# Optimization experiments

Hardware: AMD Instinct MI355X
Metric: run time of the kernel (lower is better)

The kernel has to match this reference:

```python
import jax, jax.numpy as jnp
import numpy as np

NUM_BINS = 4
SCALE = 5.0
EPS = 1e-12

def hswish(x):
    return x * jnp.clip(x + 3.0, 0.0, 6.0) / 6.0

def l2norm(x, axis):
    n = jnp.sqrt(jnp.sum(x * x, axis=axis, keepdims=True))
    return x / jnp.maximum(n, EPS)

def setup_inputs() -> dict:
    key = jax.random.key(0)
    k0, k1, k2, k3, k4 = jax.random.split(key, 5)
    B, C, T, H, W = 8, 256, 32, 28, 28
    hidden, embd = 512, 32
    x = jax.random.normal(k0, (B, C, T, H, W), dtype=jnp.float32)
    W1 = jax.random.normal(k1, (hidden, C), dtype=jnp.float32) * (1.0 / np.sqrt(C))
    b1 = jax.random.normal(k2, (hidden,), dtype=jnp.float32) * 0.01
    W2 = jax.random.normal(k3, (embd, hidden), dtype=jnp.float32) * (1.0 / np.sqrt(hidden))
    b2 = jax.random.normal(k4, (embd,), dtype=jnp.float32) * 0.01
    return {"x": x, "W1": W1, "b1": b1, "W2": W2, "b2": b2}

def reference(x, W1, b1, W2, b2):
    B, C, T, H, W = x.shape
    # encoder: global spatial avg-pool -> 1x1x1 conv -> HSwish -> 1x1x1 conv
    pooled = jnp.mean(x, axis=(3, 4))                      # (B,C,T)
    h = hswish(jnp.einsum('hc,bct->bht', W1, pooled) + b1[None, :, None])
    embds = jnp.einsum('eh,bht->bet', W2, h) + b2[None, :, None]   # (B,E,T)
    norm_embd = l2norm(embds, axis=1)

    # --- grouping (no-grad in original) ---
    ns = jnp.sum(norm_embd[:, :, 1:] * norm_embd[:, :, :-1], axis=1)    # (B,T-1)
    # k-th smallest neighbour similarity = threshold
    smallest = -jax.lax.top_k(-ns, NUM_BINS - 1)[0]                      # ascending smallest k
    threshold = smallest[:, -1]
    edges = (ns > threshold[:, None]).astype(jnp.int32)                  # (B,T-1)
    interval_ends = jnp.concatenate(
        [jnp.zeros((B, 1), dtype=jnp.int32), 1 - edges], axis=1)        # (B,T)
    groups = jnp.cumsum(interval_ends, axis=1)                           # (B,T)
    group_ids = jnp.arange(NUM_BINS, dtype=groups.dtype)
    group_mask = (groups[:, :, None] == group_ids[None, None, :]).astype(jnp.float32)  # (B,T,K)
    group_sizes = jnp.sum(group_mask, axis=1, keepdims=True)             # (B,1,K)
    centers_sum = jnp.einsum('bet,btk->bek', norm_embd, group_mask)      # (B,E,K)
    norm_centers = l2norm(centers_sum / group_sizes, axis=1)             # (B,E,K)
    norm_centers = jax.lax.stop_gradient(norm_centers)

    similarities = jnp.einsum('bet,bek->btk', norm_embd, norm_centers)   # (B,T,K)
    weights = jax.nn.softmax(SCALE * similarities, axis=2)               # (B,T,K)
    sum_weights = jnp.sum(weights, axis=1, keepdims=True)                # (B,1,K)
    scales = jnp.where(sum_weights > 0.0, 1.0 / sum_weights, jnp.ones_like(sum_weights))
    scales = jax.lax.stop_gradient(scales)
    norm_weights = scales * weights                                      # (B,T,K)

    # weighted temporal pooling: avoids (B,C,T,K,H,W) blowup
    out = jnp.einsum('bcthw,btk->bckhw', x, norm_weights)                # (B,C,K,H,W)
    return out
```

## Files before the change

### kernel.cpp

```cpp
#include <hip/hip_runtime.h>
#include <math.h>

#define BATCH 8
#define CCH   256
#define TT    32
#define HWSZ  784
#define HID   512
#define EMB   32
#define KBINS 4
#define SCALEF 5.0f
#define EPSN  1e-12f

__global__ __launch_bounds__(256) void pool_kernel(
        const float* __restrict__ x, float* __restrict__ pooled) {
    const int wave = threadIdx.x >> 6;
    const int lane = threadIdx.x & 63;
    const int row  = blockIdx.x * 4 + wave;
    const float4* xp = (const float4*)(x + (size_t)row * HWSZ);

    float4 v0 = xp[lane];
    float4 v1 = xp[lane + 64];
    float4 v2 = xp[lane + 128];
    float s = v0.x + v0.y + v0.z + v0.w
            + v1.x + v1.y + v1.z + v1.w
            + v2.x + v2.y + v2.z + v2.w;
    if (lane < 4) {
        float4 v3 = xp[lane + 192];
        s += v3.x + v3.y + v3.z + v3.w;
    }
#pragma unroll
    for (int off = 32; off > 0; off >>= 1) s += __shfl_down(s, off);
    if (lane == 0) {
        const int t = row & 31;
        const int c = (row >> 5) & 255;
        const int b = row >> 13;
        pooled[((size_t)(b * TT + t)) * CCH + c] = s * (1.0f / 784.0f);
    }
}

__global__ __launch_bounds__(512) void fc_kernel(
        const float* __restrict__ W1, const float* __restrict__ b1,
        const float* __restrict__ W2, const float* __restrict__ b2,
        const float* __restrict__ pooled, float* __restrict__ embds) {
    __shared__ float pc[CCH];
    __shared__ float hcol[HID];

    const int b = blockIdx.x >> 5;
    const int t = blockIdx.x & 31;
    const int tid = threadIdx.x;

    if (tid < CCH / 4)
        ((float4*)pc)[tid] = ((const float4*)(pooled + ((size_t)(b * TT + t)) * CCH))[tid];
    __syncthreads();

    {
        const float4* w = (const float4*)(W1 + (size_t)tid * CCH);
        float acc = 0.f;
#pragma unroll 8
        for (int j = 0; j < CCH / 4; j++) {
            float4 wv = w[j];
            acc += wv.x * pc[4 * j] + wv.y * pc[4 * j + 1]
                 + wv.z * pc[4 * j + 2] + wv.w * pc[4 * j + 3];
        }
        acc += b1[tid];
        float r = fminf(fmaxf(acc + 3.0f, 0.0f), 6.0f);
        hcol[tid] = acc * r * (1.0f / 6.0f);
    }
    __syncthreads();

    {
        const int e = tid >> 4;
        const int l = tid & 15;
        const float* w = W2 + (size_t)e * HID;
        float acc = 0.f;
#pragma unroll
        for (int j = 0; j < HID / 16; j++) acc += w[l + 16 * j] * hcol[l + 16 * j];
        acc += __shfl_down(acc, 8);
        acc += __shfl_down(acc, 4);
        acc += __shfl_down(acc, 2);
        acc += __shfl_down(acc, 1);
        if (l == 0) embds[((size_t)b * EMB + e) * TT + t] = acc + b2[e];
    }
}

__global__ void group_kernel(const float* __restrict__ embds, float* __restrict__ nw) {
    __shared__ float se[EMB][TT + 1];
    __shared__ float ns[TT];
    __shared__ float colinv[TT];
    __shared__ float thr_sh;
    __shared__ float cs[EMB][KBINS];
    __shared__ float wts[TT][KBINS];
    __shared__ float gsize[KBINS];
    __shared__ float kfac[KBINS];
    __shared__ int   gid[TT];

    const int b   = blockIdx.x;
    const int tid = threadIdx.x;

    for (int i = tid; i < EMB * TT; i += 256)
        se[i >> 5][i & 31] = embds[(size_t)b * EMB * TT + i];
    __syncthreads();

    if (tid < TT) {
        float s = 0.f;
        for (int e = 0; e < EMB; e++) { float v = se[e][tid]; s += v * v; }
        colinv[tid] = 1.0f / fmaxf(sqrtf(s), EPSN);
    }
    __syncthreads();
    for (int i = tid; i < EMB * TT; i += 256) {
        int e = i >> 5, t = i & 31;
        se[e][t] *= colinv[t];
    }
    __syncthreads();

    if (tid < TT - 1) {
        float s = 0.f;
        for (int e = 0; e < EMB; e++) s += se[e][tid] * se[e][tid + 1];
        ns[tid] = s;
    }
    __syncthreads();

    if (tid < TT - 1) {
        float v = ns[tid];
        int pos = 0;
        for (int j = 0; j < TT - 1; j++) {
            float u = ns[j];
            pos += (u < v) || (u == v && j < tid);
        }
        if (pos == KBINS - 2) thr_sh = v;
    }
    __syncthreads();

    if (tid < TT) {
        float thr = thr_sh;
        int g = 0;
        for (int s = 1; s <= tid; s++) g += !(ns[s - 1] > thr);
        gid[tid] = g;
    }
    __syncthreads();
    if (tid < KBINS) {
        float c = 0.f;
        for (int t = 0; t < TT; t++) c += (gid[t] == tid);
        gsize[tid] = c;
    }
    __syncthreads();

    if (tid < EMB * KBINS) {
        int e = tid >> 2, k = tid & 3;
        float s = 0.f;
        for (int t = 0; t < TT; t++) if (gid[t] == k) s += se[e][t];
        cs[e][k] = s / gsize[k];
    }
    __syncthreads();
    if (tid < KBINS) {
        float s = 0.f;
        for (int e = 0; e < EMB; e++) { float v = cs[e][tid]; s += v * v; }
        kfac[tid] = 1.0f / fmaxf(sqrtf(s), EPSN);
    }
    __syncthreads();
    if (tid < EMB * KBINS) {
        int e = tid >> 2, k = tid & 3;
        cs[e][k] *= kfac[k];
    }
    __syncthreads();

    if (tid < TT * KBINS) {
        int t = tid >> 2, k = tid & 3;
        float s = 0.f;
        for (int e = 0; e < EMB; e++) s += se[e][t] * cs[e][k];
        wts[t][k] = s * SCALEF;
    }
    __syncthreads();
    if (tid < TT) {
        float m = wts[tid][0];
        for (int k = 1; k < KBINS; k++) m = fmaxf(m, wts[tid][k]);
        float ex[KBINS]; float sum = 0.f;
        for (int k = 0; k < KBINS; k++) { ex[k] = expf(wts[tid][k] - m); sum += ex[k]; }
        float inv = 1.0f / sum;
        for (int k = 0; k < KBINS; k++) wts[tid][k] = ex[k] * inv;
    }
    __syncthreads();
    if (tid < KBINS) {
        float s = 0.f;
        for (int t = 0; t < TT; t++) s += wts[t][tid];
        kfac[tid] = (s > 0.f) ? (1.0f / s) : 1.0f;
    }
    __syncthreads();
    if (tid < TT * KBINS) {
        int t = tid >> 2, k = tid & 3;
        nw[((size_t)b * TT + t) * KBINS + k] = wts[t][k] * kfac[k];
    }
}

__global__ __launch_bounds__(128) void out_kernel(
        const float* __restrict__ x, const float* __restrict__ nw,
        float* __restrict__ out) {
    __shared__ float w[TT * KBINS];
    const int b = blockIdx.x / 392;
    const unsigned idx = (blockIdx.x % 392) * 128 + threadIdx.x;
    w[threadIdx.x] = nw[(size_t)b * TT * KBINS + threadIdx.x];
    __syncthreads();
    const unsigned c = idx / 196;
    const unsigned f = idx % 196;
    const float4* xp = (const float4*)(x + ((size_t)(b * CCH + c) * TT) * HWSZ);
    float4 acc[KBINS];
#pragma unroll
    for (int k = 0; k < KBINS; k++) { acc[k].x = 0.f; acc[k].y = 0.f; acc[k].z = 0.f; acc[k].w = 0.f; }
#pragma unroll 8
    for (int t = 0; t < TT; t++) {
        float4 v = xp[t * 196 + f];
#pragma unroll
        for (int k = 0; k < KBINS; k++) {
            float wk = w[t * KBINS + k];
            acc[k].x += v.x * wk;
            acc[k].y += v.y * wk;
            acc[k].z += v.z * wk;
            acc[k].w += v.w * wk;
        }
    }
    float4* op = (float4*)(out + ((size_t)(b * CCH + c) * KBINS) * HWSZ);
#pragma unroll
    for (int k = 0; k < KBINS; k++) op[k * 196 + f] = acc[k];
}

extern "C" void kernel_launch(void* const* d_in, const int* in_sizes, int n_in,
                              void* d_out, int out_size, void* d_ws, size_t ws_size,
                              hipStream_t stream) {
    const float* x  = (const float*)d_in[0];
    const float* W1 = (const float*)d_in[1];
    const float* b1 = (const float*)d_in[2];
    const float* W2 = (const float*)d_in[3];
    const float* b2 = (const float*)d_in[4];
    float* out = (float*)d_out;

    float* ws     = (float*)d_ws;
    float* pooled = ws;
    float* embds  = pooled + BATCH * TT * CCH;
    float* nw     = embds + BATCH * EMB * TT;

    pool_kernel<<<BATCH * CCH * TT / 4, 256, 0, stream>>>(x, pooled);
    fc_kernel<<<BATCH * TT, 512, 0, stream>>>(W1, b1, W2, b2, pooled, embds);
    group_kernel<<<BATCH, 256, 0, stream>>>(embds, nw);
    out_kernel<<<BATCH * 392, 128, 0, stream>>>(x, nw, out);
}
```

Measured before the change: 344.5 us.

## Fuse spatial pooling into the FC kernel and vectorize pooled reads

```diff
diff --git a/kernel.cpp b/kernel.cpp
--- a/kernel.cpp
+++ b/kernel.cpp
@@ -11,56 +11,66 @@
 #define SCALEF 5.0f
 #define EPSN  1e-12f
 
-__global__ __launch_bounds__(256) void pool_kernel(
-        const float* __restrict__ x, float* __restrict__ pooled) {
-    const int wave = threadIdx.x >> 6;
-    const int lane = threadIdx.x & 63;
-    const int row  = blockIdx.x * 4 + wave;
-    const float4* xp = (const float4*)(x + (size_t)row * HWSZ);
-
-    float4 v0 = xp[lane];
-    float4 v1 = xp[lane + 64];
-    float4 v2 = xp[lane + 128];
-    float s = v0.x + v0.y + v0.z + v0.w
-            + v1.x + v1.y + v1.z + v1.w
-            + v2.x + v2.y + v2.z + v2.w;
-    if (lane < 4) {
-        float4 v3 = xp[lane + 192];
-        s += v3.x + v3.y + v3.z + v3.w;
-    }
-#pragma unroll
-    for (int off = 32; off > 0; off >>= 1) s += __shfl_down(s, off);
-    if (lane == 0) {
-        const int t = row & 31;
-        const int c = (row >> 5) & 255;
-        const int b = row >> 13;
-        pooled[((size_t)(b * TT + t)) * CCH + c] = s * (1.0f / 784.0f);
-    }
-}
-
-__global__ __launch_bounds__(512) void fc_kernel(
+__global__ __launch_bounds__(512) void poolfc_kernel(
+        const float* __restrict__ x,
         const float* __restrict__ W1, const float* __restrict__ b1,
         const float* __restrict__ W2, const float* __restrict__ b2,
-        const float* __restrict__ pooled, float* __restrict__ embds) {
+        float* __restrict__ embds) {
     __shared__ float pc[CCH];
     __shared__ float hcol[HID];
 
-    const int b = blockIdx.x >> 5;
-    const int t = blockIdx.x & 31;
-    const int tid = threadIdx.x;
-
-    if (tid < CCH / 4)
-        ((float4*)pc)[tid] = ((const float4*)(pooled + ((size_t)(b * TT + t)) * CCH))[tid];
+    const int b    = blockIdx.x >> 5;
+    const int t    = blockIdx.x & 31;
+    const int tid  = threadIdx.x;
+    const int wave = tid >> 6;
+    const int lane = tid & 63;
+
+    const float* xbt = x + (size_t)(b * CCH) * (TT * HWSZ) + (size_t)t * HWSZ;
+#pragma unroll
+    for (int i = 0; i < 16; ++i) {
+        const int c0 = (i << 4) + wave;
+        const int c1 = c0 + 8;
+        const float4* xp0 = (const float4*)(xbt + (size_t)c0 * (TT * HWSZ));
+        const float4* xp1 = (const float4*)(xbt + (size_t)c1 * (TT * HWSZ));
+        float4 a0 = xp0[lane];
+        float4 a1 = xp0[lane + 64];
+        float4 a2 = xp0[lane + 128];
+        float4 d0 = xp1[lane];
+        float4 d1 = xp1[lane + 64];
+        float4 d2 = xp1[lane + 128];
+        float s0 = a0.x + a0.y + a0.z + a0.w
+                 + a1.x + a1.y + a1.z + a1.w
+                 + a2.x + a2.y + a2.z + a2.w;
+        float s1 = d0.x + d0.y + d0.z + d0.w
+                 + d1.x + d1.y + d1.z + d1.w
+                 + d2.x + d2.y + d2.z + d2.w;
+        if (lane < 4) {
+            float4 a3 = xp0[lane + 192];
+            float4 d3 = xp1[lane + 192];
+            s0 += a3.x + a3.y + a3.z + a3.w;
+            s1 += d3.x + d3.y + d3.z + d3.w;
+        }
+#pragma unroll
+        for (int off = 32; off > 0; off >>= 1) {
+            s0 += __shfl_down(s0, off);
+            s1 += __shfl_down(s1, off);
+        }
+        if (lane == 0) {
+            pc[c0] = s0 * (1.0f / 784.0f);
+            pc[c1] = s1 * (1.0f / 784.0f);
+        }
+    }
     __syncthreads();
 
     {
         const float4* w = (const float4*)(W1 + (size_t)tid * CCH);
+        const float4* p4 = (const float4*)pc;
         float acc = 0.f;
 #pragma unroll 8
-        for (int j = 0; j < CCH / 4; j++) {
+        for (int j = 0; j < CCH / 4; ++j) {
             float4 wv = w[j];
-            acc += wv.x * pc[4 * j] + wv.y * pc[4 * j + 1]
-                 + wv.z * pc[4 * j + 2] + wv.w * pc[4 * j + 3];
+            float4 pv = p4[j];
+            acc += wv.x * pv.x + wv.y * pv.y + wv.z * pv.z + wv.w * pv.w;
         }
         acc += b1[tid];
         float r = fminf(fmaxf(acc + 3.0f, 0.0f), 6.0f);
@@ -233,13 +243,11 @@
     const float* b2 = (const float*)d_in[4];
     float* out = (float*)d_out;
 
-    float* ws     = (float*)d_ws;
-    float* pooled = ws;
-    float* embds  = pooled + BATCH * TT * CCH;
-    float* nw     = embds + BATCH * EMB * TT;
-
-    pool_kernel<<<BATCH * CCH * TT / 4, 256, 0, stream>>>(x, pooled);
-    fc_kernel<<<BATCH * TT, 512, 0, stream>>>(W1, b1, W2, b2, pooled, embds);
+    float* ws    = (float*)d_ws;
+    float* embds = ws;
+    float* nw    = embds + BATCH * EMB * TT;
+
+    poolfc_kernel<<<BATCH * TT, 512, 0, stream>>>(x, W1, b1, W2, b2, embds);
     group_kernel<<<BATCH, 256, 0, stream>>>(embds, nw);
     out_kernel<<<BATCH * 392, 128, 0, stream>>>(x, nw, out);
 }
```

Measured after the change: 346.1 us. No clear change (+0.5%).
